# Optimization experiments

Hardware: AMD Instinct MI355X
Metric: run time of the kernel (lower is better)

## Reference

```python
import jax, jax.numpy as jnp
import numpy as np

LEAKY_ALPHA = 0.2  # tf.nn.leaky_relu default

B, N, D = 4096, 10000, 256

def setup_inputs() -> dict:
    key = jax.random.key(0)
    k1, k2, k3 = jax.random.split(key, 3)
    patient_features = jax.random.normal(k1, (B, D), dtype=jnp.float32)
    disease_nodes = jax.random.normal(k2, (N, D), dtype=jnp.float32) * 0.1
    attn_kernel = jax.random.normal(k3, (2 * D, 1), dtype=jnp.float32) * 0.05
    return {"patient_features": patient_features,
            "disease_nodes": disease_nodes,
            "attn_kernel": attn_kernel}

def reference(patient_features, disease_nodes, attn_kernel):
    # concat([patient, nodes]) @ attn_kernel == patient @ Wp + nodes @ Wn
    d = patient_features.shape[-1]
    Wp = attn_kernel[:d, 0]   # [D]
    Wn = attn_kernel[d:, 0]   # [D]
    score_p = patient_features @ Wp          # [B]
    score_n = disease_nodes @ Wn             # [N]
    scores = score_p[:, None] + score_n[None, :]      # [B, N]
    scores = jnp.where(scores >= 0, scores, LEAKY_ALPHA * scores)
    attn = jax.nn.softmax(scores, axis=1)              # softmax over nodes
    agg = jnp.einsum('bn,nd->bd', attn, disease_nodes)  # weighted sum of nodes
    return patient_features + agg
```

## Files before the change

kernel.cpp:

```cpp
#include <hip/hip_runtime.h>
#include <math.h>

#define NB 4096
#define NN 10000
#define ND 256
#define ALPHA 0.2f
#define CS 16
#define NG (NN / CS)
#define SCHUNK 25
#define NSUPER (NG / SCHUNK)
#define MSEGS 26
#define SEGLEN ((NN + MSEGS - 1) / MSEGS)
#define ZELEMS (NN + 2 * NSUPER * ND + 2 * NSUPER)

typedef unsigned long long u64;

__global__ __launch_bounds__(256) void k_dot(
    const float* __restrict__ P, const float* __restrict__ V,
    const float* __restrict__ K,
    float* __restrict__ t, float* __restrict__ s, u64* __restrict__ tk,
    int* __restrict__ zero_region) {
  int gt = blockIdx.x * 256 + threadIdx.x;
  if (gt < ZELEMS) zero_region[gt] = 0;
  int j = blockIdx.x * 4 + (threadIdx.x >> 6);
  int lane = threadIdx.x & 63;
  if (j >= NN + NB) return;
  const float* row; const float* wv; int oi; bool isn;
  if (j < NN) { row = V + (size_t)j * ND; wv = K + ND; oi = j; isn = true; }
  else        { row = P + (size_t)(j - NN) * ND; wv = K; oi = j - NN; isn = false; }
  float4 r  = ((const float4*)row)[lane];
  float4 kx = ((const float4*)wv)[lane];
  float acc = r.x * kx.x + r.y * kx.y + r.z * kx.z + r.w * kx.w;
  #pragma unroll
  for (int off = 32; off; off >>= 1) acc += __shfl_down(acc, off, 64);
  if (lane == 0) {
    if (isn) {
      t[oi] = acc;
      unsigned bits = __float_as_uint(acc);
      unsigned key = bits ^ (((int)bits >> 31) | 0x80000000u);
      tk[oi] = ((u64)key << 14) | (unsigned)oi;
    } else {
      s[oi] = acc;
    }
  }
}

__global__ __launch_bounds__(256) void k_rank(
    const u64* __restrict__ tk, int* __restrict__ rank) {
  int n = blockIdx.x * 256 + threadIdx.x;
  u64 kn = (n < NN) ? tk[n] : ~0ull;
  int m0 = blockIdx.y * SEGLEN;
  int m1 = min(NN, m0 + SEGLEN);
  int r = 0;
  int m = m0;
  #pragma unroll 1
  for (; m + 4 <= m1; m += 4) {
    u64 a = tk[m], b2 = tk[m + 1], c = tk[m + 2], dd = tk[m + 3];
    r += (a < kn) + (b2 < kn) + (c < kn) + (dd < kn);
  }
  for (; m < m1; ++m) r += (tk[m] < kn);
  if (n < NN && r) atomicAdd(&rank[n], r);
}

__global__ __launch_bounds__(256) void k_scatter(
    const float* __restrict__ t, const int* __restrict__ rank,
    float* __restrict__ tsort, float* __restrict__ eA, float* __restrict__ eC,
    int* __restrict__ idxs) {
  int n = blockIdx.x * 256 + threadIdx.x;
  if (n < NN) {
    int r = rank[n];
    float tn = t[n];
    tsort[r] = tn;
    eA[r] = __expf(tn);
    eC[r] = __expf(ALPHA * tn);
    idxs[r] = n;
  }
}

__global__ __launch_bounds__(256) void k_chunk(
    const float* __restrict__ eA, const float* __restrict__ eC,
    const int* __restrict__ idxs, const float* __restrict__ V,
    const float* __restrict__ s, const float* __restrict__ tsort,
    float* __restrict__ SA, float* __restrict__ SC,
    float* __restrict__ sa0, float* __restrict__ sc0,
    float* __restrict__ SSA, float* __restrict__ SSC,
    float* __restrict__ ssa0, float* __restrict__ ssc0,
    int* __restrict__ kk) {
  int g = blockIdx.x, d = threadIdx.x;
  if (g < NG) {
    int base = g * CS;
    float accA = 0.f, accC = 0.f, sa = 0.f, sc = 0.f;
    #pragma unroll
    for (int j = 0; j < CS; ++j) {
      int i = base + j;
      float ea = eA[i], ec = eC[i];
      float v = V[(size_t)idxs[i] * ND + d];
      accA += ea * v; accC += ec * v;
      sa += ea; sc += ec;
    }
    SA[(size_t)g * ND + d] = accA;
    SC[(size_t)g * ND + d] = accC;
    int gs = g / SCHUNK;
    atomicAdd(&SSA[(size_t)gs * ND + d], accA);
    atomicAdd(&SSC[(size_t)gs * ND + d], accC);
    if (d == 0) {
      sa0[g] = sa; sc0[g] = sc;
      atomicAdd(&ssa0[gs], sa);
      atomicAdd(&ssc0[gs], sc);
    }
  } else {
    int b = (g - NG) * 256 + d;
    float key = -s[b];
    int lo = 0, hi = NN;
    while (lo < hi) {
      int mid = (lo + hi) >> 1;
      if (tsort[mid] < key) lo = mid + 1; else hi = mid;
    }
    kk[b] = lo;
  }
}

__global__ __launch_bounds__(256) void k_finalize(
    const float* __restrict__ P, const float* __restrict__ V,
    const float* __restrict__ s, const int* __restrict__ kk,
    const float* __restrict__ eA, const float* __restrict__ eC,
    const int* __restrict__ idxs,
    const float* __restrict__ SA, const float* __restrict__ SC,
    const float* __restrict__ sa0, const float* __restrict__ sc0,
    const float* __restrict__ SSA, const float* __restrict__ SSC,
    const float* __restrict__ ssa0, const float* __restrict__ ssc0,
    float* __restrict__ out) {
  int b = blockIdx.x, d = threadIdx.x;
  int k = kk[b];
  int g = k >> 4;
  int gs = g / SCHUNK;
  float suffA = 0.f, prefC = 0.f, suffa = 0.f, prefc = 0.f;
  for (int q = gs; q < NSUPER; ++q) {
    suffA += SSA[(size_t)q * ND + d];
    suffa += ssa0[q];
  }
  for (int q = 0; q < gs; ++q) {
    prefC += SSC[(size_t)q * ND + d];
    prefc += ssc0[q];
  }
  for (int j = gs * SCHUNK; j < g; ++j) {
    suffA -= SA[(size_t)j * ND + d];
    prefC += SC[(size_t)j * ND + d];
    suffa -= sa0[j];
    prefc += sc0[j];
  }
  for (int i = g << 4; i < k; ++i) {
    float ea = eA[i], ec = eC[i];
    float v = V[(size_t)idxs[i] * ND + d];
    suffA -= ea * v; prefC += ec * v;
    suffa -= ea;     prefc += ec;
  }
  float sb = s[b];
  float ea = __expf(sb), ec = __expf(ALPHA * sb);
  float l = ea * suffa + ec * prefc;
  float agg = (ea * suffA + ec * prefC) / l;
  out[(size_t)b * ND + d] = P[(size_t)b * ND + d] + agg;
}

extern "C" void kernel_launch(void* const* d_in, const int* in_sizes, int n_in,
                              void* d_out, int out_size, void* d_ws, size_t ws_size,
                              hipStream_t stream) {
  const float* P = (const float*)d_in[0];
  const float* V = (const float*)d_in[1];
  const float* K = (const float*)d_in[2];
  float* out = (float*)d_out;

  char* w = (char*)d_ws;
  u64*   tk    = (u64*)w;   w += sizeof(u64) * NN;
  int*   zreg  = (int*)w;
  int*   rank  = (int*)w;   w += sizeof(int) * NN;
  float* SSA   = (float*)w; w += sizeof(float) * NSUPER * ND;
  float* SSC   = (float*)w; w += sizeof(float) * NSUPER * ND;
  float* ssa0  = (float*)w; w += sizeof(float) * NSUPER;
  float* ssc0  = (float*)w; w += sizeof(float) * NSUPER;
  float* t     = (float*)w; w += sizeof(float) * NN;
  float* s     = (float*)w; w += sizeof(float) * NB;
  float* tsort = (float*)w; w += sizeof(float) * NN;
  float* eA    = (float*)w; w += sizeof(float) * NN;
  float* eC    = (float*)w; w += sizeof(float) * NN;
  int*   idxs  = (int*)w;   w += sizeof(int) * NN;
  int*   kk    = (int*)w;   w += sizeof(int) * NB;
  float* SA    = (float*)w; w += sizeof(float) * (size_t)NG * ND;
  float* SC    = (float*)w; w += sizeof(float) * (size_t)NG * ND;
  float* sa0   = (float*)w; w += sizeof(float) * NG;
  float* sc0   = (float*)w; w += sizeof(float) * NG;

  k_dot<<<(NN + NB + 3) / 4, 256, 0, stream>>>(P, V, K, t, s, tk, zreg);
  k_rank<<<dim3((NN + 255) / 256, MSEGS), 256, 0, stream>>>(tk, rank);
  k_scatter<<<(NN + 255) / 256, 256, 0, stream>>>(t, rank, tsort, eA, eC, idxs);
  k_chunk<<<NG + NB / 256, 256, 0, stream>>>(eA, eC, idxs, V, s, tsort,
                                             SA, SC, sa0, sc0,
                                             SSA, SSC, ssa0, ssc0, kk);
  k_finalize<<<NB, 256, 0, stream>>>(P, V, s, kk, eA, eC, idxs,
                                     SA, SC, sa0, sc0, SSA, SSC, ssa0, ssc0, out);
}
```

Before: 127.8 us.

## Fuse rank and scatter via last-block counter; vectorize chunk and finalize with float4 per wave

Merges the rank-counting and scatter kernels into one launch. Each tile block increments a per-tile completion counter, and the last segment block to finish writes the sorted arrays. The chunk and finalize kernels now map one 64-lane wave per group or per batch row, and each lane handles a float4 across the feature dimension. This is meant to cut one launch and use wider memory accesses with fewer blocks. In exchange it adds a cross-block atomic handshake that relies on acquire/release ordering, and the per-lane atomics into the supersums become four scalar atomics each.

```diff
diff --git a/kernel.cpp b/kernel.cpp
--- a/kernel.cpp
+++ b/kernel.cpp
@@ -4,14 +4,17 @@
 #define NB 4096
 #define NN 10000
 #define ND 256
+#define ND4 (ND / 4)
 #define ALPHA 0.2f
 #define CS 16
 #define NG (NN / CS)
 #define SCHUNK 25
 #define NSUPER (NG / SCHUNK)
+#define NTILES 40
 #define MSEGS 26
 #define SEGLEN ((NN + MSEGS - 1) / MSEGS)
-#define ZELEMS (NN + 2 * NSUPER * ND + 2 * NSUPER)
+#define CHUNK_BLOCKS ((NG + 3) / 4)
+#define ZELEMS (NN + NTILES + 2 * NSUPER * ND + 2 * NSUPER)
 
 typedef unsigned long long u64;
 
@@ -45,12 +48,15 @@
   }
 }
 
-__global__ __launch_bounds__(256) void k_rank(
-    const u64* __restrict__ tk, int* __restrict__ rank) {
-  int n = blockIdx.x * 256 + threadIdx.x;
+__global__ __launch_bounds__(256) void k_rank_scatter(
+    const u64* __restrict__ tk, const float* __restrict__ t,
+    int* __restrict__ rank, int* __restrict__ ntdone,
+    float* __restrict__ tsort, float* __restrict__ eA, float* __restrict__ eC,
+    int* __restrict__ idxs) {
+  int ntile = blockIdx.x, seg = blockIdx.y;
+  int n = ntile * 256 + threadIdx.x;
   u64 kn = (n < NN) ? tk[n] : ~0ull;
-  int m0 = blockIdx.y * SEGLEN;
-  int m1 = min(NN, m0 + SEGLEN);
+  int m0 = seg * SEGLEN, m1 = min(NN, m0 + SEGLEN);
   int r = 0;
   int m = m0;
   #pragma unroll 1
@@ -60,20 +66,20 @@
   }
   for (; m < m1; ++m) r += (tk[m] < kn);
   if (n < NN && r) atomicAdd(&rank[n], r);
-}
-
-__global__ __launch_bounds__(256) void k_scatter(
-    const float* __restrict__ t, const int* __restrict__ rank,
-    float* __restrict__ tsort, float* __restrict__ eA, float* __restrict__ eC,
-    int* __restrict__ idxs) {
-  int n = blockIdx.x * 256 + threadIdx.x;
-  if (n < NN) {
-    int r = rank[n];
+  __syncthreads();
+  __shared__ int who;
+  if (threadIdx.x == 0)
+    who = __hip_atomic_fetch_add(&ntdone[ntile], 1, __ATOMIC_ACQ_REL,
+                                 __HIP_MEMORY_SCOPE_AGENT);
+  __syncthreads();
+  if (who == MSEGS - 1 && n < NN) {
+    int rr = __hip_atomic_load(&rank[n], __ATOMIC_RELAXED,
+                               __HIP_MEMORY_SCOPE_AGENT);
     float tn = t[n];
-    tsort[r] = tn;
-    eA[r] = __expf(tn);
-    eC[r] = __expf(ALPHA * tn);
-    idxs[r] = n;
+    tsort[rr] = tn;
+    eA[rr] = __expf(tn);
+    eC[rr] = __expf(ALPHA * tn);
+    idxs[rr] = n;
   }
 }
 
@@ -86,37 +92,50 @@
     float* __restrict__ SSA, float* __restrict__ SSC,
     float* __restrict__ ssa0, float* __restrict__ ssc0,
     int* __restrict__ kk) {
-  int g = blockIdx.x, d = threadIdx.x;
-  if (g < NG) {
+  int bid = blockIdx.x, tid = threadIdx.x;
+  if (bid < CHUNK_BLOCKS) {
+    int g = bid * 4 + (tid >> 6);
+    if (g >= NG) return;
+    int lane = tid & 63;
+    const float4* V4 = (const float4*)V;
+    float4 aA = {0.f, 0.f, 0.f, 0.f}, aC = {0.f, 0.f, 0.f, 0.f};
+    float sa = 0.f, sc = 0.f;
     int base = g * CS;
-    float accA = 0.f, accC = 0.f, sa = 0.f, sc = 0.f;
     #pragma unroll
     for (int j = 0; j < CS; ++j) {
       int i = base + j;
       float ea = eA[i], ec = eC[i];
-      float v = V[(size_t)idxs[i] * ND + d];
-      accA += ea * v; accC += ec * v;
+      int id = idxs[i];
+      float4 v = V4[(size_t)id * ND4 + lane];
+      aA.x += ea * v.x; aA.y += ea * v.y; aA.z += ea * v.z; aA.w += ea * v.w;
+      aC.x += ec * v.x; aC.y += ec * v.y; aC.z += ec * v.z; aC.w += ec * v.w;
       sa += ea; sc += ec;
     }
-    SA[(size_t)g * ND + d] = accA;
-    SC[(size_t)g * ND + d] = accC;
+    ((float4*)SA)[(size_t)g * ND4 + lane] = aA;
+    ((float4*)SC)[(size_t)g * ND4 + lane] = aC;
     int gs = g / SCHUNK;
-    atomicAdd(&SSA[(size_t)gs * ND + d], accA);
-    atomicAdd(&SSC[(size_t)gs * ND + d], accC);
-    if (d == 0) {
+    float* pA = &SSA[(size_t)gs * ND + lane * 4];
+    float* pC = &SSC[(size_t)gs * ND + lane * 4];
+    atomicAdd(pA + 0, aA.x); atomicAdd(pA + 1, aA.y);
+    atomicAdd(pA + 2, aA.z); atomicAdd(pA + 3, aA.w);
+    atomicAdd(pC + 0, aC.x); atomicAdd(pC + 1, aC.y);
+    atomicAdd(pC + 2, aC.z); atomicAdd(pC + 3, aC.w);
+    if (lane == 0) {
       sa0[g] = sa; sc0[g] = sc;
       atomicAdd(&ssa0[gs], sa);
       atomicAdd(&ssc0[gs], sc);
     }
   } else {
-    int b = (g - NG) * 256 + d;
-    float key = -s[b];
-    int lo = 0, hi = NN;
-    while (lo < hi) {
-      int mid = (lo + hi) >> 1;
-      if (tsort[mid] < key) lo = mid + 1; else hi = mid;
-    }
-    kk[b] = lo;
+    int b = (bid - CHUNK_BLOCKS) * 256 + tid;
+    if (b < NB) {
+      float key = -s[b];
+      int lo = 0, hi = NN;
+      while (lo < hi) {
+        int mid = (lo + hi) >> 1;
+        if (tsort[mid] < key) lo = mid + 1; else hi = mid;
+      }
+      kk[b] = lo;
+    }
   }
 }
 
@@ -130,36 +149,52 @@
     const float* __restrict__ SSA, const float* __restrict__ SSC,
     const float* __restrict__ ssa0, const float* __restrict__ ssc0,
     float* __restrict__ out) {
-  int b = blockIdx.x, d = threadIdx.x;
+  int b = blockIdx.x * 4 + (threadIdx.x >> 6);
+  int lane = threadIdx.x & 63;
   int k = kk[b];
   int g = k >> 4;
   int gs = g / SCHUNK;
-  float suffA = 0.f, prefC = 0.f, suffa = 0.f, prefc = 0.f;
+  const float4* SSA4 = (const float4*)SSA;
+  const float4* SSC4 = (const float4*)SSC;
+  const float4* SA4  = (const float4*)SA;
+  const float4* SC4  = (const float4*)SC;
+  const float4* V4   = (const float4*)V;
+  float4 sA = {0.f, 0.f, 0.f, 0.f}, pC = {0.f, 0.f, 0.f, 0.f};
+  float suffa = 0.f, prefc = 0.f;
   for (int q = gs; q < NSUPER; ++q) {
-    suffA += SSA[(size_t)q * ND + d];
+    float4 v = SSA4[(size_t)q * ND4 + lane];
+    sA.x += v.x; sA.y += v.y; sA.z += v.z; sA.w += v.w;
     suffa += ssa0[q];
   }
   for (int q = 0; q < gs; ++q) {
-    prefC += SSC[(size_t)q * ND + d];
+    float4 v = SSC4[(size_t)q * ND4 + lane];
+    pC.x += v.x; pC.y += v.y; pC.z += v.z; pC.w += v.w;
     prefc += ssc0[q];
   }
   for (int j = gs * SCHUNK; j < g; ++j) {
-    suffA -= SA[(size_t)j * ND + d];
-    prefC += SC[(size_t)j * ND + d];
-    suffa -= sa0[j];
-    prefc += sc0[j];
+    float4 a = SA4[(size_t)j * ND4 + lane];
+    float4 c = SC4[(size_t)j * ND4 + lane];
+    sA.x -= a.x; sA.y -= a.y; sA.z -= a.z; sA.w -= a.w;
+    pC.x += c.x; pC.y += c.y; pC.z += c.z; pC.w += c.w;
+    suffa -= sa0[j]; prefc += sc0[j];
   }
   for (int i = g << 4; i < k; ++i) {
     float ea = eA[i], ec = eC[i];
-    float v = V[(size_t)idxs[i] * ND + d];
-    suffA -= ea * v; prefC += ec * v;
-    suffa -= ea;     prefc += ec;
+    float4 v = V4[(size_t)idxs[i] * ND4 + lane];
+    sA.x -= ea * v.x; sA.y -= ea * v.y; sA.z -= ea * v.z; sA.w -= ea * v.w;
+    pC.x += ec * v.x; pC.y += ec * v.y; pC.z += ec * v.z; pC.w += ec * v.w;
+    suffa -= ea; prefc += ec;
   }
   float sb = s[b];
   float ea = __expf(sb), ec = __expf(ALPHA * sb);
-  float l = ea * suffa + ec * prefc;
-  float agg = (ea * suffA + ec * prefC) / l;
-  out[(size_t)b * ND + d] = P[(size_t)b * ND + d] + agg;
+  float inv = 1.f / (ea * suffa + ec * prefc);
+  float4 p = ((const float4*)P)[(size_t)b * ND4 + lane];
+  float4 o;
+  o.x = p.x + (ea * sA.x + ec * pC.x) * inv;
+  o.y = p.y + (ea * sA.y + ec * pC.y) * inv;
+  o.z = p.z + (ea * sA.z + ec * pC.z) * inv;
+  o.w = p.w + (ea * sA.w + ec * pC.w) * inv;
+  ((float4*)out)[(size_t)b * ND4 + lane] = o;
 }
 
 extern "C" void kernel_launch(void* const* d_in, const int* in_sizes, int n_in,
@@ -174,6 +209,7 @@
   u64*   tk    = (u64*)w;   w += sizeof(u64) * NN;
   int*   zreg  = (int*)w;
   int*   rank  = (int*)w;   w += sizeof(int) * NN;
+  int*   ntdone= (int*)w;   w += sizeof(int) * NTILES;
   float* SSA   = (float*)w; w += sizeof(float) * NSUPER * ND;
   float* SSC   = (float*)w; w += sizeof(float) * NSUPER * ND;
   float* ssa0  = (float*)w; w += sizeof(float) * NSUPER;
@@ -191,11 +227,10 @@
   float* sc0   = (float*)w; w += sizeof(float) * NG;
 
   k_dot<<<(NN + NB + 3) / 4, 256, 0, stream>>>(P, V, K, t, s, tk, zreg);
-  k_rank<<<dim3((NN + 255) / 256, MSEGS), 256, 0, stream>>>(tk, rank);
-  k_scatter<<<(NN + 255) / 256, 256, 0, stream>>>(t, rank, tsort, eA, eC, idxs);
-  k_chunk<<<NG + NB / 256, 256, 0, stream>>>(eA, eC, idxs, V, s, tsort,
-                                             SA, SC, sa0, sc0,
-                                             SSA, SSC, ssa0, ssc0, kk);
-  k_finalize<<<NB, 256, 0, stream>>>(P, V, s, kk, eA, eC, idxs,
-                                     SA, SC, sa0, sc0, SSA, SSC, ssa0, ssc0, out);
-}
+  k_rank_scatter<<<dim3(NTILES, MSEGS), 256, 0, stream>>>(
+      tk, t, rank, ntdone, tsort, eA, eC, idxs);
+  k_chunk<<<CHUNK_BLOCKS + NB / 256, 256, 0, stream>>>(
+      eA, eC, idxs, V, s, tsort, SA, SC, sa0, sc0, SSA, SSC, ssa0, ssc0, kk);
+  k_finalize<<<NB / 4, 256, 0, stream>>>(
+      P, V, s, kk, eA, eC, idxs, SA, SC, sa0, sc0, SSA, SSC, ssa0, ssc0, out);
+}
```

Result: slower. 134.6 us (+5.3%).

## Fuse rank and scatter via last-block counter; batch finalize rows with shared prefix sums

Applied to the files above, without the earlier changes.

The rank and scatter kernels are merged: every segment block atomically bumps a per-tile counter, and the last block for a tile does the scatter after an acquire fence, which removes one launch. The finalize kernel now handles 8 batch rows per block and first builds prefix sums of the super-chunk partials in shared memory, so each row does O(1) lookups instead of looping over super-chunks. The cost is fewer finalize blocks (512), which lowers parallelism, plus reliance on correct cross-block memory ordering for the scatter.

```diff
diff --git a/kernel.cpp b/kernel.cpp
--- a/kernel.cpp
+++ b/kernel.cpp
@@ -9,9 +9,11 @@
 #define NG (NN / CS)
 #define SCHUNK 25
 #define NSUPER (NG / SCHUNK)
+#define NTILES 40
 #define MSEGS 26
 #define SEGLEN ((NN + MSEGS - 1) / MSEGS)
-#define ZELEMS (NN + 2 * NSUPER * ND + 2 * NSUPER)
+#define FPB 8
+#define ZELEMS (NN + NTILES + 2 * NSUPER * ND + 2 * NSUPER)
 
 typedef unsigned long long u64;
 
@@ -45,35 +47,40 @@
   }
 }
 
-__global__ __launch_bounds__(256) void k_rank(
-    const u64* __restrict__ tk, int* __restrict__ rank) {
-  int n = blockIdx.x * 256 + threadIdx.x;
+__global__ __launch_bounds__(256) void k_rank_scatter(
+    const u64* __restrict__ tk, const float* __restrict__ t,
+    int* __restrict__ rank, int* __restrict__ ntdone,
+    float* __restrict__ tsort, float* __restrict__ eA, float* __restrict__ eC,
+    int* __restrict__ idxs) {
+  int ntile = blockIdx.x, seg = blockIdx.y;
+  int n = ntile * 256 + threadIdx.x;
   u64 kn = (n < NN) ? tk[n] : ~0ull;
-  int m0 = blockIdx.y * SEGLEN;
-  int m1 = min(NN, m0 + SEGLEN);
+  int m0 = seg * SEGLEN, m1 = min(NN, m0 + SEGLEN);
   int r = 0;
   int m = m0;
   #pragma unroll 1
   for (; m + 4 <= m1; m += 4) {
-    u64 a = tk[m], b2 = tk[m + 1], c = tk[m + 2], dd = tk[m + 3];
-    r += (a < kn) + (b2 < kn) + (c < kn) + (dd < kn);
-  }
-  for (; m < m1; ++m) r += (tk[m] < kn);
+    u64 a = tk[m], b2 = tk[m + 1], c2 = tk[m + 2], d2 = tk[m + 3];
+    r += (int)(a < kn) + (int)(b2 < kn) + (int)(c2 < kn) + (int)(d2 < kn);
+  }
+  for (; m < m1; ++m) r += (int)(tk[m] < kn);
   if (n < NN && r) atomicAdd(&rank[n], r);
-}
-
-__global__ __launch_bounds__(256) void k_scatter(
-    const float* __restrict__ t, const int* __restrict__ rank,
-    float* __restrict__ tsort, float* __restrict__ eA, float* __restrict__ eC,
-    int* __restrict__ idxs) {
-  int n = blockIdx.x * 256 + threadIdx.x;
-  if (n < NN) {
-    int r = rank[n];
-    float tn = t[n];
-    tsort[r] = tn;
-    eA[r] = __expf(tn);
-    eC[r] = __expf(ALPHA * tn);
-    idxs[r] = n;
+  __syncthreads();
+  __shared__ int who;
+  if (threadIdx.x == 0)
+    who = __hip_atomic_fetch_add(&ntdone[ntile], 1, __ATOMIC_ACQ_REL,
+                                 __HIP_MEMORY_SCOPE_AGENT);
+  __syncthreads();
+  if (who == MSEGS - 1) {
+    __builtin_amdgcn_fence(__ATOMIC_ACQUIRE, "agent");
+    if (n < NN) {
+      int rr = rank[n];
+      float tn = t[n];
+      tsort[rr] = tn;
+      eA[rr] = __expf(tn);
+      eC[rr] = __expf(ALPHA * tn);
+      idxs[rr] = n;
+    }
   }
 }
 
@@ -110,13 +117,15 @@
     }
   } else {
     int b = (g - NG) * 256 + d;
-    float key = -s[b];
-    int lo = 0, hi = NN;
-    while (lo < hi) {
-      int mid = (lo + hi) >> 1;
-      if (tsort[mid] < key) lo = mid + 1; else hi = mid;
-    }
-    kk[b] = lo;
+    if (b < NB) {
+      float key = -s[b];
+      int lo = 0, hi = NN;
+      while (lo < hi) {
+        int mid = (lo + hi) >> 1;
+        if (tsort[mid] < key) lo = mid + 1; else hi = mid;
+      }
+      kk[b] = lo;
+    }
   }
 }
 
@@ -130,36 +139,54 @@
     const float* __restrict__ SSA, const float* __restrict__ SSC,
     const float* __restrict__ ssa0, const float* __restrict__ ssc0,
     float* __restrict__ out) {
-  int b = blockIdx.x, d = threadIdx.x;
-  int k = kk[b];
-  int g = k >> 4;
-  int gs = g / SCHUNK;
-  float suffA = 0.f, prefC = 0.f, suffa = 0.f, prefc = 0.f;
-  for (int q = gs; q < NSUPER; ++q) {
-    suffA += SSA[(size_t)q * ND + d];
-    suffa += ssa0[q];
-  }
-  for (int q = 0; q < gs; ++q) {
-    prefC += SSC[(size_t)q * ND + d];
-    prefc += ssc0[q];
-  }
-  for (int j = gs * SCHUNK; j < g; ++j) {
-    suffA -= SA[(size_t)j * ND + d];
-    prefC += SC[(size_t)j * ND + d];
-    suffa -= sa0[j];
-    prefc += sc0[j];
-  }
-  for (int i = g << 4; i < k; ++i) {
-    float ea = eA[i], ec = eC[i];
-    float v = V[(size_t)idxs[i] * ND + d];
-    suffA -= ea * v; prefC += ec * v;
-    suffa -= ea;     prefc += ec;
-  }
-  float sb = s[b];
-  float ea = __expf(sb), ec = __expf(ALPHA * sb);
-  float l = ea * suffa + ec * prefc;
-  float agg = (ea * suffA + ec * prefC) / l;
-  out[(size_t)b * ND + d] = P[(size_t)b * ND + d] + agg;
+  __shared__ float lpsa[(NSUPER + 1) * ND];
+  __shared__ float lpsc[(NSUPER + 1) * ND];
+  __shared__ float lpa0[NSUPER + 1], lpc0[NSUPER + 1];
+  int d = threadIdx.x;
+  float runA = 0.f, runC = 0.f;
+  lpsa[d] = 0.f; lpsc[d] = 0.f;
+  for (int q = 0; q < NSUPER; ++q) {
+    runA += SSA[(size_t)q * ND + d];
+    runC += SSC[(size_t)q * ND + d];
+    lpsa[(q + 1) * ND + d] = runA;
+    lpsc[(q + 1) * ND + d] = runC;
+  }
+  if (d == 0) {
+    float ra = 0.f, rc = 0.f;
+    lpa0[0] = 0.f; lpc0[0] = 0.f;
+    for (int q = 0; q < NSUPER; ++q) {
+      ra += ssa0[q]; rc += ssc0[q];
+      lpa0[q + 1] = ra; lpc0[q + 1] = rc;
+    }
+  }
+  __syncthreads();
+  #pragma unroll 1
+  for (int p = 0; p < FPB; ++p) {
+    int b = blockIdx.x * FPB + p;
+    int k = kk[b];
+    int g = k >> 4;
+    int gs = g / SCHUNK;
+    float suffA = lpsa[NSUPER * ND + d] - lpsa[gs * ND + d];
+    float prefC = lpsc[gs * ND + d];
+    float suffa = lpa0[NSUPER] - lpa0[gs];
+    float prefc = lpc0[gs];
+    for (int j = gs * SCHUNK; j < g; ++j) {
+      suffA -= SA[(size_t)j * ND + d];
+      prefC += SC[(size_t)j * ND + d];
+      suffa -= sa0[j]; prefc += sc0[j];
+    }
+    for (int i = g << 4; i < k; ++i) {
+      float ea = eA[i], ec = eC[i];
+      float v = V[(size_t)idxs[i] * ND + d];
+      suffA -= ea * v; prefC += ec * v;
+      suffa -= ea; prefc += ec;
+    }
+    float sb = s[b];
+    float ea = __expf(sb), ec = __expf(ALPHA * sb);
+    float inv = 1.f / (ea * suffa + ec * prefc);
+    out[(size_t)b * ND + d] = P[(size_t)b * ND + d] +
+                              (ea * suffA + ec * prefC) * inv;
+  }
 }
 
 extern "C" void kernel_launch(void* const* d_in, const int* in_sizes, int n_in,
@@ -174,6 +201,7 @@
   u64*   tk    = (u64*)w;   w += sizeof(u64) * NN;
   int*   zreg  = (int*)w;
   int*   rank  = (int*)w;   w += sizeof(int) * NN;
+  int*   ntdone= (int*)w;   w += sizeof(int) * NTILES;
   float* SSA   = (float*)w; w += sizeof(float) * NSUPER * ND;
   float* SSC   = (float*)w; w += sizeof(float) * NSUPER * ND;
   float* ssa0  = (float*)w; w += sizeof(float) * NSUPER;
@@ -191,11 +219,10 @@
   float* sc0   = (float*)w; w += sizeof(float) * NG;
 
   k_dot<<<(NN + NB + 3) / 4, 256, 0, stream>>>(P, V, K, t, s, tk, zreg);
-  k_rank<<<dim3((NN + 255) / 256, MSEGS), 256, 0, stream>>>(tk, rank);
-  k_scatter<<<(NN + 255) / 256, 256, 0, stream>>>(t, rank, tsort, eA, eC, idxs);
-  k_chunk<<<NG + NB / 256, 256, 0, stream>>>(eA, eC, idxs, V, s, tsort,
-                                             SA, SC, sa0, sc0,
-                                             SSA, SSC, ssa0, ssc0, kk);
-  k_finalize<<<NB, 256, 0, stream>>>(P, V, s, kk, eA, eC, idxs,
-                                     SA, SC, sa0, sc0, SSA, SSC, ssa0, ssc0, out);
-}
+  k_rank_scatter<<<dim3(NTILES, MSEGS), 256, 0, stream>>>(
+      tk, t, rank, ntdone, tsort, eA, eC, idxs);
+  k_chunk<<<NG + NB / 256, 256, 0, stream>>>(
+      eA, eC, idxs, V, s, tsort, SA, SC, sa0, sc0, SSA, SSC, ssa0, ssc0, kk);
+  k_finalize<<<NB / FPB, 256, 0, stream>>>(
+      P, V, s, kk, eA, eC, idxs, SA, SC, sa0, sc0, SSA, SSC, ssa0, ssc0, out);
+}
```

Measured after the change: 145.7 us. 1.14x slower.
